# Optimization experiments

Hardware: AMD Instinct MI355X
Metric: run time of the kernel (lower is better)

## Reference

```python
import jax, jax.numpy as jnp
import numpy as np
from jax import lax

EPS = 1e-5
DN = ('NCHW', 'OIHW', 'NCHW')

@jax.custom_vjp
def binact(x):
    # XNOR-Net BinActive: sign forward, STE backward (grad zeroed where |x|>1)
    return jnp.sign(x)

def _binact_fwd(x):
    return jnp.sign(x), x

def _binact_bwd(x, g):
    return (g * (jnp.abs(x) <= 1).astype(g.dtype),)

binact.defvjp(_binact_fwd, _binact_bwd)

def bn(x, gamma, beta, mean, var):
    scale = gamma * lax.rsqrt(var + EPS)
    return x * scale[None, :, None, None] + (beta - mean * scale)[None, :, None, None]

def conv(x, w, stride=1, pad=0):
    return lax.conv_general_dilated(x, w, (stride, stride), [(pad, pad), (pad, pad)],
                                    dimension_numbers=DN)

def setup_inputs() -> dict:
    key = jax.random.key(0)
    ks = jax.random.split(key, 16)
    inplanes, planes = 1024, 256
    d = {}
    d['x'] = jax.random.normal(ks[0], (64, inplanes, 14, 14), jnp.float32)
    d['bn1_gamma'] = jax.random.uniform(ks[1], (inplanes,), jnp.float32)
    d['bn1_beta'] = jax.random.normal(ks[2], (inplanes,), jnp.float32)
    d['bn1_mean'] = jax.random.normal(ks[3], (inplanes,), jnp.float32)
    d['bn1_var'] = jax.random.uniform(ks[4], (inplanes,), jnp.float32)
    d['W1'] = jax.random.normal(ks[5], (planes, inplanes, 1, 1), jnp.float32) * 0.05
    d['bn2_gamma'] = jax.random.uniform(ks[6], (planes,), jnp.float32)
    d['bn2_beta'] = jax.random.normal(ks[7], (planes,), jnp.float32)
    d['bn2_mean'] = jax.random.normal(ks[8], (planes,), jnp.float32)
    d['bn2_var'] = jax.random.uniform(ks[9], (planes,), jnp.float32)
    d['W2'] = jax.random.normal(ks[10], (planes, planes, 3, 3), jnp.float32) * 0.05
    d['bn3_gamma'] = jax.random.uniform(ks[11], (planes,), jnp.float32)
    d['bn3_beta'] = jax.random.normal(ks[12], (planes,), jnp.float32)
    d['bn3_mean'] = jax.random.normal(ks[13], (planes,), jnp.float32)
    d['bn3_var'] = jax.random.uniform(ks[14], (planes,), jnp.float32)
    d['W3'] = jax.random.normal(ks[15], (planes * 4, planes, 1, 1), jnp.float32) * 0.05
    return d

def reference(x, bn1_gamma, bn1_beta, bn1_mean, bn1_var, W1,
              bn2_gamma, bn2_beta, bn2_mean, bn2_var, W2,
              bn3_gamma, bn3_beta, bn3_mean, bn3_var, W3):
    residual = x
    h = binact(bn(x, bn1_gamma, bn1_beta, bn1_mean, bn1_var))
    h = jax.nn.relu(conv(h, W1))                      # 1x1
    h = binact(bn(h, bn2_gamma, bn2_beta, bn2_mean, bn2_var))
    h = jax.nn.relu(conv(h, W2, stride=1, pad=1))     # 3x3
    h = binact(bn(h, bn3_gamma, bn3_beta, bn3_mean, bn3_var))
    h = conv(h, W3)                                   # 1x1 expansion
    return jax.nn.relu(h + residual)
```

## Files before the change

kernel.cpp:

```cpp
#include <hip/hip_runtime.h>

#define EPS 1e-5f

typedef __attribute__((ext_vector_type(8))) short bf16x8;
typedef __attribute__((ext_vector_type(4))) float f32x4;

#define MFMA16(a, b, c) __builtin_amdgcn_mfma_f32_16x16x32_bf16(a, b, c, 0, 0, 0)

__device__ __forceinline__ void gl16(const void* g, void* l) {
    __builtin_amdgcn_global_load_lds(
        (const __attribute__((address_space(1))) unsigned int*)g,
        (__attribute__((address_space(3))) unsigned int*)l, 16, 0, 0);
}

__device__ __forceinline__ unsigned short f2bf(float f) {
    unsigned u = __float_as_uint(f);
    unsigned r = (u + 0x7FFFu + ((u >> 16) & 1u)) >> 16;
    return (unsigned short)r;
}
__device__ __forceinline__ float bf2f(unsigned short h) {
    return __uint_as_float(((unsigned)h) << 16);
}


__global__ __launch_bounds__(256, 2) void k_pre(
    const float* __restrict__ x,
    const float* __restrict__ g1, const float* __restrict__ be1,
    const float* __restrict__ mu1, const float* __restrict__ va1,
    const float* __restrict__ W1,
    const float* __restrict__ g2, const float* __restrict__ be2,
    const float* __restrict__ mu2, const float* __restrict__ va2,
    const float* __restrict__ W2,
    const float* __restrict__ g3, const float* __restrict__ be3,
    const float* __restrict__ mu3, const float* __restrict__ va3,
    const float* __restrict__ W3,
    unsigned short* __restrict__ A1, unsigned short* __restrict__ A2,
    unsigned short* __restrict__ A3,
    float* __restrict__ sc2, float* __restrict__ sh2,
    float* __restrict__ sc3, float* __restrict__ sh3,
    unsigned short* __restrict__ b1, unsigned short* __restrict__ b2p)
{
    __shared__ unsigned short tile[128 * 197];
    __shared__ float ssc[128], ssh[128];
    const int wg = blockIdx.x;
    const int tid = threadIdx.x;

    if (wg < 512) {
        const int n = wg >> 3, c0 = (wg & 7) * 128;
        if (tid < 128) {
            int c = c0 + tid;
            float sc = g1[c] * (1.0f / sqrtf(va1[c] + EPS));
            ssc[tid] = sc;
            ssh[tid] = be1[c] - mu1[c] * sc;
        }
        __syncthreads();
        const float4* xp4 = (const float4*)(x + ((size_t)n * 1024 + c0) * 196);
        for (int it = 0; it < 25; ++it) {
            int e = it * 256 + tid;
            if (e < 6272) {
                int c = e / 49, q = e - c * 49, p = q * 4;
                float4 xv = xp4[e];
                float sc = ssc[c], sh = ssh[c];
                float t0 = xv.x * sc + sh, t1 = xv.y * sc + sh;
                float t2 = xv.z * sc + sh, t3 = xv.w * sc + sh;
                unsigned short* tp = &tile[c * 197 + p];
                tp[0] = (t0 > 0.f) ? 0x3F80 : ((t0 < 0.f) ? 0xBF80 : 0);
                tp[1] = (t1 > 0.f) ? 0x3F80 : ((t1 < 0.f) ? 0xBF80 : 0);
                tp[2] = (t2 > 0.f) ? 0x3F80 : ((t2 < 0.f) ? 0xBF80 : 0);
                tp[3] = (t3 > 0.f) ? 0x3F80 : ((t3 < 0.f) ? 0xBF80 : 0);
            }
        }
        __syncthreads();
        const int pr = tid >> 4, cg = (tid & 15) * 8;
        for (int it = 0; it < 13; ++it) {
            int p = it * 16 + pr;
            if (p < 196) {
                unsigned short vals[8];
                #pragma unroll
                for (int j = 0; j < 8; ++j) vals[j] = tile[(cg + j) * 197 + p];
                uint4 pk;
                pk.x = (unsigned)vals[0] | ((unsigned)vals[1] << 16);
                pk.y = (unsigned)vals[2] | ((unsigned)vals[3] << 16);
                pk.z = (unsigned)vals[4] | ((unsigned)vals[5] << 16);
                pk.w = (unsigned)vals[6] | ((unsigned)vals[7] << 16);
                *(uint4*)&b1[((size_t)n * 196 + p) * 1024 + c0 + cg] = pk;
            }
        }
    } else if (wg < 2816) {
        int i = (wg - 512) * 256 + tid;
        if (i < 262144) {
            float w = W1[i];
            unsigned short h1 = f2bf(w); float r1 = w - bf2f(h1);
            unsigned short h2 = f2bf(r1); float r2 = r1 - bf2f(h2);
            unsigned short h3 = f2bf(r2);
            A1[i] = h1; A1[262144 + i] = h2; A1[524288 + i] = h3;
            A3[i] = f2bf(W3[i]);
        }
        {
            int co = i / 2304, k = i - co * 2304;
            int ci = k / 9, tap = k - ci * 9;
            int o = co * 2304 + tap * 256 + ci;
            float w = W2[i];
            unsigned short h1 = f2bf(w); float r1 = w - bf2f(h1);
            unsigned short h2 = f2bf(r1); float r2 = r1 - bf2f(h2);
            unsigned short h3 = f2bf(r2);
            A2[o] = h1; A2[589824 + o] = h2; A2[1179648 + o] = h3;
        }
        if (i < 256) {
            float s2 = g2[i] * (1.0f / sqrtf(va2[i] + EPS));
            sc2[i] = s2; sh2[i] = be2[i] - mu2[i] * s2;
            float s3 = g3[i] * (1.0f / sqrtf(va3[i] + EPS));
            sc3[i] = s3; sh3[i] = be3[i] - mu3[i] * s3;
        }
    } else {
        int t = (wg - 2816) * 256 + tid;
        if (t < 122880) {
            int ci8 = t & 31;
            int tb = t >> 5;
            int bidx = tb % 60, n = tb / 60;
            int sp;
            if (bidx < 16) sp = bidx;
            else if (bidx < 32) sp = 240 + (bidx - 16);
            else { int s2 = bidx - 32; sp = ((s2 >> 1) + 1) * 16 + (s2 & 1) * 15; }
            ulonglong2 z; z.x = 0; z.y = 0;
            *(ulonglong2*)&b2p[((size_t)(n * 256 + sp)) * 256 + ci8 * 8] = z;
        }
    }
}

__global__ __launch_bounds__(256, 2) void k_gemm1(
    const unsigned short* __restrict__ A1, const unsigned short* __restrict__ B1,
    const float* __restrict__ sc2, const float* __restrict__ sh2,
    unsigned short* __restrict__ b2p)
{
    __shared__ unsigned short sA[2][3][2048];
    __shared__ unsigned short sB[2][4096];
    const int tid = threadIdx.x;
    const int wg = blockIdx.x;
    const int r = (wg & 7) * 49 + (wg >> 3);
    const int co0 = (r & 3) * 64;
    const int m0  = (r >> 2) * 128;
    const int lane = tid & 63, w = tid >> 6;
    const int wr = w & 1, wc = w >> 1;
    const int srow = tid >> 2;
    const int sq = (tid & 3) ^ ((tid >> 3) & 3);
    const int frow = lane & 15;
    const int fq = (lane >> 4) ^ ((frow >> 1) & 3);

    const unsigned short* gA  = A1 + (size_t)(co0 + srow) * 1024 + sq * 8;
    const unsigned short* gB0 = B1 + (size_t)(m0 + srow) * 1024 + sq * 8;
    const unsigned short* gB1 = B1 + (size_t)(m0 + 64 + srow) * 1024 + sq * 8;

    auto STAGE = [&](int t, int c) {
        int k0 = t << 5;
        gl16(gA + k0,          &sA[c][0][tid * 8]);
        gl16(gA + 262144 + k0, &sA[c][1][tid * 8]);
        gl16(gA + 524288 + k0, &sA[c][2][tid * 8]);
        gl16(gB0 + k0, &sB[c][tid * 8]);
        gl16(gB1 + k0, &sB[c][2048 + tid * 8]);
    };

    f32x4 acc[2][4];
    #pragma unroll
    for (int i = 0; i < 2; ++i)
        #pragma unroll
        for (int j = 0; j < 4; ++j) acc[i][j] = (f32x4){0.f, 0.f, 0.f, 0.f};

    STAGE(0, 0);
    __syncthreads();
    int cur = 0;
    for (int t = 0; t < 32; ++t) {
        if (t < 31) STAGE(t + 1, cur ^ 1);
        bf16x8 af[3][2], bfr[4];
        #pragma unroll
        for (int s = 0; s < 3; ++s)
            #pragma unroll
            for (int fr = 0; fr < 2; ++fr)
                af[s][fr] = *(const bf16x8*)&sA[cur][s][(wr * 32 + fr * 16 + frow) * 32 + fq * 8];
        #pragma unroll
        for (int fc = 0; fc < 4; ++fc)
            bfr[fc] = *(const bf16x8*)&sB[cur][(wc * 64 + fc * 16 + frow) * 32 + fq * 8];
        #pragma unroll
        for (int s = 0; s < 3; ++s)
            #pragma unroll
            for (int fr = 0; fr < 2; ++fr)
                #pragma unroll
                for (int fc = 0; fc < 4; ++fc)
                    acc[fr][fc] = MFMA16(af[s][fr], bfr[fc], acc[fr][fc]);
        __syncthreads();
        cur ^= 1;
    }
    #pragma unroll
    for (int fc = 0; fc < 4; ++fc) {
        int m = m0 + wc * 64 + fc * 16 + frow;
        int n = m / 196, p = m - n * 196;
        int y = p / 14, xx = p - y * 14;
        size_t ob = ((size_t)(n * 256 + (y + 1) * 16 + (xx + 1))) * 256;
        #pragma unroll
        for (int fr = 0; fr < 2; ++fr) {
            int co = co0 + wr * 32 + fr * 16 + (lane >> 4) * 4;
            unsigned short o[4];
            #pragma unroll
            for (int q = 0; q < 4; ++q) {
                float h = fmaxf(acc[fr][fc][q], 0.f);
                float t = h * sc2[co + q] + sh2[co + q];
                o[q] = (t > 0.f) ? 0x3F80 : ((t < 0.f) ? 0xBF80 : 0);
            }
            ushort4 pk; pk.x = o[0]; pk.y = o[1]; pk.z = o[2]; pk.w = o[3];
            *(ushort4*)&b2p[ob + co] = pk;
        }
    }
}

__global__ __launch_bounds__(256, 2) void k_gemm2(
    const unsigned short* __restrict__ A2, const unsigned short* __restrict__ b2p,
    const float* __restrict__ sc3, const float* __restrict__ sh3,
    unsigned short* __restrict__ b3)
{
    __shared__ unsigned short sA[2][3][2048];
    __shared__ unsigned short sB[2][4096];
    const int tid = threadIdx.x;
    const int wg = blockIdx.x;
    const int r = (wg & 7) * 64 + (wg >> 3);
    const int co0 = (r & 3) * 64;
    const int m0  = (r >> 2) * 128;
    const int nB  = m0 >> 8;
    const int sp0 = m0 & 255;
    const int lane = tid & 63, w = tid >> 6;
    const int wr = w & 1, wc = w >> 1;
    const int srow = tid >> 2;
    const int sq = (tid & 3) ^ ((tid >> 3) & 3);
    const int frow = lane & 15;
    const int fq = (lane >> 4) ^ ((frow >> 1) & 3);

    const long bbase = (long)(nB * 256 + sp0) * 256;

    auto STAGE = [&](int t, int c) {
        int tap = t >> 3, ci0 = (t & 7) << 5;
        int dy = (tap * 11) >> 5, dx = tap - dy * 3;
        int toff = (dy - 1) * 16 + dx - 1;
        const unsigned short* gA = A2 + (size_t)(co0 + srow) * 2304 + tap * 256 + ci0 + sq * 8;
        gl16(gA,           &sA[c][0][tid * 8]);
        gl16(gA + 589824,  &sA[c][1][tid * 8]);
        gl16(gA + 1179648, &sA[c][2][tid * 8]);
        long boff = bbase + (long)(toff + srow) * 256 + ci0 + sq * 8;
        gl16(b2p + boff,             &sB[c][tid * 8]);
        gl16(b2p + boff + 64 * 256,  &sB[c][2048 + tid * 8]);
    };

    f32x4 acc[2][4];
    #pragma unroll
    for (int i = 0; i < 2; ++i)
        #pragma unroll
        for (int j = 0; j < 4; ++j) acc[i][j] = (f32x4){0.f, 0.f, 0.f, 0.f};

    STAGE(0, 0);
    __syncthreads();
    int cur = 0;
    for (int t = 0; t < 72; ++t) {
        if (t < 71) STAGE(t + 1, cur ^ 1);
        bf16x8 af[3][2], bfr[4];
        #pragma unroll
        for (int s = 0; s < 3; ++s)
            #pragma unroll
            for (int fr = 0; fr < 2; ++fr)
                af[s][fr] = *(const bf16x8*)&sA[cur][s][(wr * 32 + fr * 16 + frow) * 32 + fq * 8];
        #pragma unroll
        for (int fc = 0; fc < 4; ++fc)
            bfr[fc] = *(const bf16x8*)&sB[cur][(wc * 64 + fc * 16 + frow) * 32 + fq * 8];
        #pragma unroll
        for (int s = 0; s < 3; ++s)
            #pragma unroll
            for (int fr = 0; fr < 2; ++fr)
                #pragma unroll
                for (int fc = 0; fc < 4; ++fc)
                    acc[fr][fc] = MFMA16(af[s][fr], bfr[fc], acc[fr][fc]);
        __syncthreads();
        cur ^= 1;
    }
    #pragma unroll
    for (int fc = 0; fc < 4; ++fc) {
        int m = m0 + wc * 64 + fc * 16 + frow;
        int sp = m & 255, nn = m >> 8;
        int y = sp >> 4, xx = sp & 15;
        if (y >= 1 && y <= 14 && xx >= 1 && xx <= 14) {
            int p = (y - 1) * 14 + (xx - 1);
            size_t ob = ((size_t)nn * 196 + p) * 256;
            #pragma unroll
            for (int fr = 0; fr < 2; ++fr) {
                int co = co0 + wr * 32 + fr * 16 + (lane >> 4) * 4;
                unsigned short o[4];
                #pragma unroll
                for (int q = 0; q < 4; ++q) {
                    float h = fmaxf(acc[fr][fc][q], 0.f);
                    float t = h * sc3[co + q] + sh3[co + q];
                    o[q] = (t > 0.f) ? 0x3F80 : ((t < 0.f) ? 0xBF80 : 0);
                }
                ushort4 pk; pk.x = o[0]; pk.y = o[1]; pk.z = o[2]; pk.w = o[3];
                *(ushort4*)&b3[ob + co] = pk;
            }
        }
    }
}

__global__ __launch_bounds__(256, 3) void k_gemm3(
    const unsigned short* __restrict__ A3, const unsigned short* __restrict__ B3,
    const float* __restrict__ xres, float* __restrict__ out)
{
    __shared__ unsigned short sA[2][4096];
    __shared__ unsigned short sB[2][4096];
    const int tid = threadIdx.x;
    const int wg = blockIdx.x;
    const int r = (wg & 7) * 98 + (wg >> 3);
    const int co0 = (r & 7) * 128;
    const int m0  = (r >> 3) * 128;
    const int lane = tid & 63, w = tid >> 6;
    const int wr = w >> 1, wc = w & 1;
    const int srow = tid >> 2;
    const int sq = (tid & 3) ^ ((tid >> 3) & 3);
    const int frow = lane & 15;
    const int fq = (lane >> 4) ^ ((frow >> 1) & 3);

    auto STAGE = [&](int t, int c) {
        int k0 = t << 5;
        gl16(A3 + (size_t)(co0 + srow) * 256 + k0 + sq * 8,      &sA[c][tid * 8]);
        gl16(A3 + (size_t)(co0 + 64 + srow) * 256 + k0 + sq * 8, &sA[c][2048 + tid * 8]);
        gl16(B3 + (size_t)(m0 + srow) * 256 + k0 + sq * 8,       &sB[c][tid * 8]);
        gl16(B3 + (size_t)(m0 + 64 + srow) * 256 + k0 + sq * 8,  &sB[c][2048 + tid * 8]);
    };

    f32x4 acc[4][4];
    #pragma unroll
    for (int i = 0; i < 4; ++i)
        #pragma unroll
        for (int j = 0; j < 4; ++j) acc[i][j] = (f32x4){0.f, 0.f, 0.f, 0.f};

    STAGE(0, 0);
    __syncthreads();
    int cur = 0;
    for (int t = 0; t < 8; ++t) {
        if (t < 7) STAGE(t + 1, cur ^ 1);
        bf16x8 af[4], bfr[4];
        #pragma unroll
        for (int fr = 0; fr < 4; ++fr)
            af[fr] = *(const bf16x8*)&sA[cur][(wr * 64 + fr * 16 + frow) * 32 + fq * 8];
        #pragma unroll
        for (int fc = 0; fc < 4; ++fc)
            bfr[fc] = *(const bf16x8*)&sB[cur][(wc * 64 + fc * 16 + frow) * 32 + fq * 8];
        #pragma unroll
        for (int fr = 0; fr < 4; ++fr)
            #pragma unroll
            for (int fc = 0; fc < 4; ++fc)
                acc[fr][fc] = MFMA16(af[fr], bfr[fc], acc[fr][fc]);
        __syncthreads();
        cur ^= 1;
    }
    #pragma unroll
    for (int fc = 0; fc < 4; ++fc) {
        int m = m0 + wc * 64 + fc * 16 + frow;
        int n = m / 196, p = m - n * 196;
        #pragma unroll
        for (int fr = 0; fr < 4; ++fr) {
            int co = co0 + wr * 64 + fr * 16 + (lane >> 4) * 4;
            size_t idx = ((size_t)n * 1024 + co) * 196 + p;
            #pragma unroll
            for (int q = 0; q < 4; ++q)
                out[idx + (size_t)q * 196] =
                    fmaxf(acc[fr][fc][q] + xres[idx + (size_t)q * 196], 0.f);
        }
    }
}

extern "C" void kernel_launch(void* const* d_in, const int* in_sizes, int n_in,
                              void* d_out, int out_size, void* d_ws, size_t ws_size,
                              hipStream_t stream) {
    const float* x   = (const float*)d_in[0];
    const float* g1  = (const float*)d_in[1];
    const float* be1 = (const float*)d_in[2];
    const float* mu1 = (const float*)d_in[3];
    const float* va1 = (const float*)d_in[4];
    const float* W1  = (const float*)d_in[5];
    const float* g2  = (const float*)d_in[6];
    const float* be2 = (const float*)d_in[7];
    const float* mu2 = (const float*)d_in[8];
    const float* va2 = (const float*)d_in[9];
    const float* W2  = (const float*)d_in[10];
    const float* g3  = (const float*)d_in[11];
    const float* be3 = (const float*)d_in[12];
    const float* mu3 = (const float*)d_in[13];
    const float* va3 = (const float*)d_in[14];
    const float* W3  = (const float*)d_in[15];
    float* out = (float*)d_out;

    char* p = (char*)d_ws;
    unsigned short* A1 = (unsigned short*)p;  p += 3 * 262144 * 2;
    unsigned short* A2 = (unsigned short*)p;  p += 3 * 589824 * 2;
    unsigned short* A3 = (unsigned short*)p;  p += 262144 * 2;
    float* sc2 = (float*)p;                   p += 256 * 4;
    float* sh2 = (float*)p;                   p += 256 * 4;
    float* sc3 = (float*)p;                   p += 256 * 4;
    float* sh3 = (float*)p;                   p += 256 * 4;
    unsigned short* b1 = (unsigned short*)p;  p += (size_t)12544 * 1024 * 2;
    p += 16384;
    unsigned short* b2p = (unsigned short*)p; p += (size_t)64 * 256 * 256 * 2;
    p += 16384;
    unsigned short* b3 = (unsigned short*)p;

    k_pre<<<3296, 256, 0, stream>>>(x, g1, be1, mu1, va1, W1,
                                    g2, be2, mu2, va2, W2,
                                    g3, be3, mu3, va3, W3,
                                    A1, A2, A3, sc2, sh2, sc3, sh3, b1, b2p);
    k_gemm1<<<392, 256, 0, stream>>>(A1, b1, sc2, sh2, b2p);
    k_gemm2<<<512, 256, 0, stream>>>(A2, b2p, sc3, sh3, b3);
    k_gemm3<<<784, 256, 0, stream>>>(A3, b3, x, out);
}
```

Baseline: 267.1 us.

## Triple-buffer GEMM LDS stages with explicit vmcnt waits and raw barriers

```diff
diff --git a/kernel.cpp b/kernel.cpp
--- a/kernel.cpp
+++ b/kernel.cpp
@@ -133,8 +133,8 @@
     const float* __restrict__ sc2, const float* __restrict__ sh2,
     unsigned short* __restrict__ b2p)
 {
-    __shared__ unsigned short sA[2][3][2048];
-    __shared__ unsigned short sB[2][4096];
+    __shared__ unsigned short sA[3][3][2048];
+    __shared__ unsigned short sB[3][4096];
     const int tid = threadIdx.x;
     const int wg = blockIdx.x;
     const int r = (wg & 7) * 49 + (wg >> 3);
@@ -167,10 +167,19 @@
         for (int j = 0; j < 4; ++j) acc[i][j] = (f32x4){0.f, 0.f, 0.f, 0.f};
 
     STAGE(0, 0);
-    __syncthreads();
+    STAGE(1, 1);
     int cur = 0;
     for (int t = 0; t < 32; ++t) {
-        if (t < 31) STAGE(t + 1, cur ^ 1);
+        if (t < 30) {
+            int stg = cur + 2; if (stg >= 3) stg -= 3;
+            STAGE(t + 2, stg);
+            asm volatile("s_waitcnt vmcnt(10)" ::: "memory");
+        } else if (t == 30) {
+            asm volatile("s_waitcnt vmcnt(5)" ::: "memory");
+        } else {
+            asm volatile("s_waitcnt vmcnt(0)" ::: "memory");
+        }
+        __builtin_amdgcn_s_barrier();
         bf16x8 af[3][2], bfr[4];
         #pragma unroll
         for (int s = 0; s < 3; ++s)
@@ -187,8 +196,8 @@
                 #pragma unroll
                 for (int fc = 0; fc < 4; ++fc)
                     acc[fr][fc] = MFMA16(af[s][fr], bfr[fc], acc[fr][fc]);
-        __syncthreads();
-        cur ^= 1;
+        __builtin_amdgcn_s_barrier();
+        cur = (cur == 2) ? 0 : cur + 1;
     }
     #pragma unroll
     for (int fc = 0; fc < 4; ++fc) {
@@ -217,8 +226,8 @@
     const float* __restrict__ sc3, const float* __restrict__ sh3,
     unsigned short* __restrict__ b3)
 {
-    __shared__ unsigned short sA[2][3][2048];
-    __shared__ unsigned short sB[2][4096];
+    __shared__ unsigned short sA[3][3][2048];
+    __shared__ unsigned short sB[3][4096];
     const int tid = threadIdx.x;
     const int wg = blockIdx.x;
     const int r = (wg & 7) * 64 + (wg >> 3);
@@ -255,10 +264,19 @@
         for (int j = 0; j < 4; ++j) acc[i][j] = (f32x4){0.f, 0.f, 0.f, 0.f};
 
     STAGE(0, 0);
-    __syncthreads();
+    STAGE(1, 1);
     int cur = 0;
     for (int t = 0; t < 72; ++t) {
-        if (t < 71) STAGE(t + 1, cur ^ 1);
+        if (t < 70) {
+            int stg = cur + 2; if (stg >= 3) stg -= 3;
+            STAGE(t + 2, stg);
+            asm volatile("s_waitcnt vmcnt(10)" ::: "memory");
+        } else if (t == 70) {
+            asm volatile("s_waitcnt vmcnt(5)" ::: "memory");
+        } else {
+            asm volatile("s_waitcnt vmcnt(0)" ::: "memory");
+        }
+        __builtin_amdgcn_s_barrier();
         bf16x8 af[3][2], bfr[4];
         #pragma unroll
         for (int s = 0; s < 3; ++s)
@@ -275,8 +293,8 @@
                 #pragma unroll
                 for (int fc = 0; fc < 4; ++fc)
                     acc[fr][fc] = MFMA16(af[s][fr], bfr[fc], acc[fr][fc]);
-        __syncthreads();
-        cur ^= 1;
+        __builtin_amdgcn_s_barrier();
+        cur = (cur == 2) ? 0 : cur + 1;
     }
     #pragma unroll
     for (int fc = 0; fc < 4; ++fc) {
@@ -307,8 +325,8 @@
     const unsigned short* __restrict__ A3, const unsigned short* __restrict__ B3,
     const float* __restrict__ xres, float* __restrict__ out)
 {
-    __shared__ unsigned short sA[2][4096];
-    __shared__ unsigned short sB[2][4096];
+    __shared__ unsigned short sA[3][4096];
+    __shared__ unsigned short sB[3][4096];
     const int tid = threadIdx.x;
     const int wg = blockIdx.x;
     const int r = (wg & 7) * 98 + (wg >> 3);
@@ -336,10 +354,19 @@
         for (int j = 0; j < 4; ++j) acc[i][j] = (f32x4){0.f, 0.f, 0.f, 0.f};
 
     STAGE(0, 0);
-    __syncthreads();
+    STAGE(1, 1);
     int cur = 0;
     for (int t = 0; t < 8; ++t) {
-        if (t < 7) STAGE(t + 1, cur ^ 1);
+        if (t < 6) {
+            int stg = cur + 2; if (stg >= 3) stg -= 3;
+            STAGE(t + 2, stg);
+            asm volatile("s_waitcnt vmcnt(8)" ::: "memory");
+        } else if (t == 6) {
+            asm volatile("s_waitcnt vmcnt(4)" ::: "memory");
+        } else {
+            asm volatile("s_waitcnt vmcnt(0)" ::: "memory");
+        }
+        __builtin_amdgcn_s_barrier();
         bf16x8 af[4], bfr[4];
         #pragma unroll
         for (int fr = 0; fr < 4; ++fr)
@@ -352,8 +379,8 @@
             #pragma unroll
             for (int fc = 0; fc < 4; ++fc)
                 acc[fr][fc] = MFMA16(af[fr], bfr[fc], acc[fr][fc]);
-        __syncthreads();
-        cur ^= 1;
+        __builtin_amdgcn_s_barrier();
+        cur = (cur == 2) ? 0 : cur + 1;
     }
     #pragma unroll
     for (int fc = 0; fc < 4; ++fc) {
```

Result: faster. 254.1 us (-4.9%).
